# Kernel optimization log

Measured on AMD Instinct MI355X. Metric: run time of the kernel, lower is better.

The kernel has to match this reference:

```python
import jax, jax.numpy as jnp
import numpy as np

D_MODEL = 1024
N_HEADS = 16
HEAD_DIM = D_MODEL // N_HEADS
N_EXPERTS = 8
TOP_K = 2
D_FF = 4096
B, T = 4, 1024
EPS = 1e-5


def setup_inputs() -> dict:
    key = jax.random.key(0)
    ks = jax.random.split(key, 12)
    s = lambda fan_in: 1.0 / np.sqrt(fan_in)
    x = jax.random.normal(ks[0], (B, T, D_MODEL), dtype=jnp.float32)
    # additive causal mask (0 on/below diagonal, -inf above)
    mask = jnp.where(jnp.tril(jnp.ones((T, T), dtype=bool)), 0.0, -1e9).astype(jnp.float32)
    return {
        "x": x,
        "mask": mask,
        "ln1_g": jnp.ones((D_MODEL,), jnp.float32),
        "ln1_b": jnp.zeros((D_MODEL,), jnp.float32),
        "w_qkv": jax.random.normal(ks[1], (D_MODEL, 3 * D_MODEL), jnp.float32) * s(D_MODEL),
        "w_proj": jax.random.normal(ks[2], (D_MODEL, D_MODEL), jnp.float32) * s(D_MODEL),
        "b_proj": jnp.zeros((D_MODEL,), jnp.float32),
        "ln2_g": jnp.ones((D_MODEL,), jnp.float32),
        "ln2_b": jnp.zeros((D_MODEL,), jnp.float32),
        "w_router": jax.random.normal(ks[3], (D_MODEL, N_EXPERTS), jnp.float32) * s(D_MODEL),
        "w1": jax.random.normal(ks[4], (N_EXPERTS, D_MODEL, D_FF), jnp.float32) * s(D_MODEL),
        "b1": jnp.zeros((N_EXPERTS, D_FF), jnp.float32),
        "w2": jax.random.normal(ks[5], (N_EXPERTS, D_FF, D_MODEL), jnp.float32) * s(D_FF),
        "b2": jnp.zeros((N_EXPERTS, D_MODEL), jnp.float32),
    }


def _layer_norm(x, g, b):
    mu = jnp.mean(x, axis=-1, keepdims=True)
    var = jnp.var(x, axis=-1, keepdims=True)
    return (x - mu) * jax.lax.rsqrt(var + EPS) * g + b


def _rope(q, k):
    # q, k: [B, H, T, hd]; GPT-NeoX half-split rotary
    t = q.shape[2]
    half = HEAD_DIM // 2
    inv_freq = 1.0 / (10000.0 ** (jnp.arange(0, half, dtype=jnp.float32) / half))
    ang = jnp.arange(t, dtype=jnp.float32)[:, None] * inv_freq[None, :]  # [T, half]
    cos = jnp.concatenate([jnp.cos(ang), jnp.cos(ang)], axis=-1)[None, None]  # [1,1,T,hd]
    sin = jnp.concatenate([jnp.sin(ang), jnp.sin(ang)], axis=-1)[None, None]

    def rot_half(u):
        u1, u2 = jnp.split(u, 2, axis=-1)
        return jnp.concatenate([-u2, u1], axis=-1)

    return q * cos + rot_half(q) * sin, k * cos + rot_half(k) * sin


def _attention(x, mask, w_qkv, w_proj, b_proj):
    b, t, _ = x.shape
    qkv = x @ w_qkv  # [B,T,3D]
    q, k, v = jnp.split(qkv, 3, axis=-1)
    rs = lambda u: u.reshape(b, t, N_HEADS, HEAD_DIM).transpose(0, 2, 1, 3)
    q, k, v = rs(q), rs(k), rs(v)
    q, k = _rope(q, k)
    scale = HEAD_DIM ** -0.5
    scores = jnp.einsum("bhqd,bhkd->bhqk", q, k) * scale + mask
    attn = jax.nn.softmax(scores, axis=-1)
    out = jnp.einsum("bhqk,bhkd->bhqd", attn, v)
    out = out.transpose(0, 2, 1, 3).reshape(b, t, D_MODEL)
    return out @ w_proj + b_proj


def _moe(x, w_router, w1, b1, w2, b2):
    b, t, d = x.shape
    xf = x.reshape(-1, d)  # [N, d]
    logits = xf @ w_router  # [N, E]
    probs = jax.nn.softmax(logits, axis=-1)
    top_v, top_i = jax.lax.top_k(probs, TOP_K)  # [N, k]
    weights = top_v / jnp.sum(top_v, axis=-1, keepdims=True)
    onehot = jax.nn.one_hot(top_i, N_EXPERTS, dtype=xf.dtype)  # [N, k, E]
    gates = jnp.einsum("nk,nke->ne", weights, onehot)  # [N, E]
    # dense grouped-FFN over experts
    h = jax.nn.gelu(jnp.einsum("nd,edf->enf", xf, w1) + b1[:, None, :], approximate=False)
    y = jnp.einsum("enf,efd->end", h, w2) + b2[:, None, :]
    out = jnp.einsum("end,ne->nd", y, gates).reshape(b, t, d)
    # load-balancing aux loss (Switch-style)
    dispatch = jnp.sum(onehot, axis=1)  # [N, E]
    frac = jnp.mean(dispatch, axis=0) / TOP_K
    mean_prob = jnp.mean(probs, axis=0)
    aux = N_EXPERTS * jnp.sum(frac * mean_prob)
    return out, aux


def reference(x, mask, ln1_g, ln1_b, w_qkv, w_proj, b_proj, ln2_g, ln2_b,
              w_router, w1, b1, w2, b2):
    # dropout is identity (eval / p=0)
    x = x + _attention(_layer_norm(x, ln1_g, ln1_b), mask, w_qkv, w_proj, b_proj)
    moe_out, aux = _moe(_layer_norm(x, ln2_g, ln2_b), w_router, w1, b1, w2, b2)
    x = x + moe_out
    return x, aux
```

## Files before the change

kernel.cpp:

```cpp
#include <hip/hip_runtime.h>
#include <math.h>


typedef __bf16 bf16;
typedef __bf16 bf16x8 __attribute__((ext_vector_type(8)));
typedef float  f32x4  __attribute__((ext_vector_type(4)));

#define D_MODEL 1024
#define SEQ     1024
#define NTOK    4096
#define DFF     4096
#define NEXP    8

__device__ __forceinline__ f32x4 mfma16(bf16x8 a, bf16x8 b, f32x4 c) {
  return __builtin_amdgcn_mfma_f32_16x16x32_bf16(a, b, c, 0, 0, 0);
}

__device__ __forceinline__ void async_cp16(void* lds, const void* g) {
  __builtin_amdgcn_global_load_lds(
      (__attribute__((address_space(1))) void*)(void*)g,
      (__attribute__((address_space(3))) void*)lds, 16, 0, 0);
}

__device__ __forceinline__ int swz(int row, int col) {
  return row * 64 + (col ^ (((row ^ (row >> 3)) & 7) << 3));
}

template<bool SPLIT>
__device__ __forceinline__ void gemm_core(
    const bf16* __restrict__ Ahi, const bf16* __restrict__ Alo,
    const bf16* __restrict__ Bhi, const bf16* __restrict__ Blo,
    long aOff0, long aOff1, long bOff0, long bOff1,
    int K, bf16* As, bf16* Bs, f32x4 acc[4][4])
{
  const int tid  = threadIdx.x;
  const int lane = tid & 63, w = tid >> 6;
  const int fr   = lane & 15, quad = lane >> 4;
  const int wm   = w >> 1,    wn   = w & 1;
  bf16* AsD0 = As + (w * 16) * 32;
  bf16* AsD1 = As + (64 + w * 16) * 32;
  bf16* BsD0 = Bs + (w * 16) * 32;
  bf16* BsD1 = Bs + (64 + w * 16) * 32;
  const int nph = SPLIT ? 3 : 1;
  for (int ph = 0; ph < nph; ++ph) {
    const bf16* Ap = (ph == 1) ? Alo : Ahi;
    const bf16* Bp = (ph == 2) ? Blo : Bhi;
    for (int k0 = 0; k0 < K; k0 += 32) {
      async_cp16(AsD0, Ap + aOff0 + k0);
      async_cp16(AsD1, Ap + aOff1 + k0);
      async_cp16(BsD0, Bp + bOff0 + k0);
      async_cp16(BsD1, Bp + bOff1 + k0);
      __syncthreads();
      bf16x8 af[4], bfv[4];
#pragma unroll
      for (int mi = 0; mi < 4; ++mi)
        af[mi] = *(const bf16x8*)&As[(wm * 64 + mi * 16 + fr) * 32 + quad * 8];
#pragma unroll
      for (int ni = 0; ni < 4; ++ni)
        bfv[ni] = *(const bf16x8*)&Bs[(wn * 64 + ni * 16 + fr) * 32 + quad * 8];
#pragma unroll
      for (int mi = 0; mi < 4; ++mi)
#pragma unroll
        for (int ni = 0; ni < 4; ++ni)
          acc[mi][ni] = mfma16(af[mi], bfv[ni], acc[mi][ni]);
      __syncthreads();
    }
  }
}

__global__ void k_transpose_cast(const float* __restrict__ in,
                                 bf16* __restrict__ oh, bf16* __restrict__ ol,
                                 int K, int N)
{
  const long zo = (long)blockIdx.z * K * N;
  __shared__ float tile[32][33];
  const int tx = threadIdx.x & 31, ty = threadIdx.x >> 5;
  const int r0 = blockIdx.y * 32, c0 = blockIdx.x * 32;
#pragma unroll
  for (int j = 0; j < 4; ++j)
    tile[ty + 8 * j][tx] = in[zo + (long)(r0 + ty + 8 * j) * N + (c0 + tx)];
  __syncthreads();
#pragma unroll
  for (int j = 0; j < 4; ++j) {
    float v = tile[tx][ty + 8 * j];
    long  o = zo + (long)(c0 + ty + 8 * j) * K + (r0 + tx);
    bf16 hh = (bf16)v;
    oh[o] = hh;
    if (ol) ol[o] = (bf16)(v - (float)hh);
  }
}

__global__ __launch_bounds__(256) void k_layernorm(
    const float* __restrict__ x, const float* __restrict__ g,
    const float* __restrict__ b, bf16* __restrict__ oh, bf16* __restrict__ ol)
{
  const int tok = blockIdx.x, tid = threadIdx.x;
  const float4 v = ((const float4*)(x + (long)tok * D_MODEL))[tid];
  float s  = v.x + v.y + v.z + v.w;
  float s2 = v.x * v.x + v.y * v.y + v.z * v.z + v.w * v.w;
#pragma unroll
  for (int off = 1; off < 64; off <<= 1) {
    s  += __shfl_xor(s, off);
    s2 += __shfl_xor(s2, off);
  }
  __shared__ float red[8];
  if ((tid & 63) == 0) { red[tid >> 6] = s; red[4 + (tid >> 6)] = s2; }
  __syncthreads();
  s  = red[0] + red[1] + red[2] + red[3];
  s2 = red[4] + red[5] + red[6] + red[7];
  const float mu   = s * (1.0f / D_MODEL);
  const float var  = s2 * (1.0f / D_MODEL) - mu * mu;
  const float rstd = 1.0f / sqrtf(var + 1e-5f);
  const float4 gg = ((const float4*)g)[tid];
  const float4 bb = ((const float4*)b)[tid];
  float o0 = (v.x - mu) * rstd * gg.x + bb.x;
  float o1 = (v.y - mu) * rstd * gg.y + bb.y;
  float o2 = (v.z - mu) * rstd * gg.z + bb.z;
  float o3 = (v.w - mu) * rstd * gg.w + bb.w;
  const long base = (long)tok * D_MODEL + tid * 4;
  bf16 h0 = (bf16)o0, h1 = (bf16)o1, h2 = (bf16)o2, h3 = (bf16)o3;
  oh[base + 0] = h0; oh[base + 1] = h1; oh[base + 2] = h2; oh[base + 3] = h3;
  if (ol) {
    ol[base + 0] = (bf16)(o0 - (float)h0);
    ol[base + 1] = (bf16)(o1 - (float)h1);
    ol[base + 2] = (bf16)(o2 - (float)h2);
    ol[base + 3] = (bf16)(o3 - (float)h3);
  }
}

__global__ __launch_bounds__(256, 2) void k_gemm_qkv(
    const bf16* __restrict__ Ah, const bf16* __restrict__ Al,
    const bf16* __restrict__ Bh, const bf16* __restrict__ Bl,
    float* __restrict__ out)
{
  __shared__ __align__(16) bf16 As[128 * 32];
  __shared__ __align__(16) bf16 Bs[128 * 32];
  const int tid = threadIdx.x, lane = tid & 63, w = tid >> 6;
  const int fr = lane & 15, quad = lane >> 4;
  const int wm = w >> 1, wn = w & 1;
  const int m0 = blockIdx.y * 128, n0 = blockIdx.x * 128;
  const int lrow = w * 16 + (lane >> 2), colk = (lane & 3) * 8;
  long aOff0 = (long)(m0 + lrow) * D_MODEL + colk;
  long aOff1 = aOff0 + 64L * D_MODEL;
  long bOff0 = (long)(n0 + lrow) * D_MODEL + colk;
  long bOff1 = bOff0 + 64L * D_MODEL;
  f32x4 acc[4][4];
  f32x4 zv = {0.f, 0.f, 0.f, 0.f};
#pragma unroll
  for (int i = 0; i < 4; ++i)
#pragma unroll
    for (int j = 0; j < 4; ++j) acc[i][j] = zv;
  gemm_core<true>(Ah, Al, Bh, Bl, aOff0, aOff1, bOff0, bOff1, D_MODEL, As, Bs, acc);
#pragma unroll
  for (int mi = 0; mi < 4; ++mi)
#pragma unroll
    for (int ni = 0; ni < 4; ++ni) {
      const int col = n0 + wn * 64 + ni * 16 + fr;
#pragma unroll
      for (int r = 0; r < 4; ++r) {
        const int row = m0 + wm * 64 + mi * 16 + quad * 4 + r;
        out[(long)row * 3072 + col] = acc[mi][ni][r];
      }
    }
}

__global__ __launch_bounds__(256) void k_rope(
    const float* __restrict__ qkv,
    bf16* __restrict__ qh, bf16* __restrict__ ql,
    bf16* __restrict__ kh, bf16* __restrict__ kl,
    bf16* __restrict__ vh, bf16* __restrict__ vl)
{
  const int tok = blockIdx.x;
  const int t = tok & (SEQ - 1), bb = tok >> 10;
  const int tid = threadIdx.x;
  const float ft = (float)t;
  for (int it = tid; it < 512; it += 256) {
    const int hh = it >> 5, i = it & 31;
    const float inv = powf(10000.0f, -(float)i * (1.0f / 32.0f));
    const float ang = ft * inv;
    float sn, cs;
    sincosf(ang, &sn, &cs);
    const long src = (long)tok * 3072 + hh * 64 + i;
    const float q0 = qkv[src], q1 = qkv[src + 32];
    const float k0 = qkv[src + 1024], k1 = qkv[src + 1024 + 32];
    const float qo0 = q0 * cs - q1 * sn, qo1 = q1 * cs + q0 * sn;
    const float ko0 = k0 * cs - k1 * sn, ko1 = k1 * cs + k0 * sn;
    const long dst = ((long)(bb * 16 + hh) * SEQ + t) * 64 + i;
    bf16 x;
    x = (bf16)qo0; qh[dst] = x;      ql[dst] = (bf16)(qo0 - (float)x);
    x = (bf16)qo1; qh[dst + 32] = x; ql[dst + 32] = (bf16)(qo1 - (float)x);
    x = (bf16)ko0; kh[dst] = x;      kl[dst] = (bf16)(ko0 - (float)x);
    x = (bf16)ko1; kh[dst + 32] = x; kl[dst + 32] = (bf16)(ko1 - (float)x);
  }
  for (int it = tid; it < 1024; it += 256) {
    const int hh = it >> 6, d = it & 63;
    const float vv = qkv[(long)tok * 3072 + 2048 + it];
    const long dst = ((long)(bb * 16 + hh) * SEQ + t) * 64 + d;
    bf16 x = (bf16)vv;
    vh[dst] = x; vl[dst] = (bf16)(vv - (float)x);
  }
}

__global__ __launch_bounds__(256, 3) void k_flash(
    const bf16* __restrict__ qh, const bf16* __restrict__ ql,
    const bf16* __restrict__ kh, const bf16* __restrict__ kl,
    const bf16* __restrict__ vh, const bf16* __restrict__ vl,
    bf16* __restrict__ oh, bf16* __restrict__ ol)
{
  const int qt = blockIdx.x, bhid = blockIdx.y;
  const int tid = threadIdx.x, lane = tid & 63, w = tid >> 6;
  const int fr = lane & 15, quad = lane >> 4;
  __shared__ __align__(16) bf16 QP0[64 * 64];
  __shared__ __align__(16) bf16 QP1[64 * 64];
  __shared__ __align__(16) bf16 Kh[64 * 64], Kl[64 * 64];
  __shared__ __align__(16) bf16 Vh[64 * 64], Vl[64 * 64];

  const long qbase = ((long)bhid * SEQ + qt * 64) * 64;
  for (int c = tid; c < 512; c += 256) {
    const int row = c >> 3, c8 = (c & 7) << 3;
    *(uint4*)&QP0[swz(row, c8)] = *(const uint4*)&qh[qbase + row * 64 + c8];
    *(uint4*)&QP1[swz(row, c8)] = *(const uint4*)&ql[qbase + row * 64 + c8];
  }
  __syncthreads();
  bf16x8 aQh[2], aQl[2];
#pragma unroll
  for (int kk = 0; kk < 2; ++kk) {
    aQh[kk] = *(const bf16x8*)&QP0[swz(w * 16 + fr, kk * 32 + quad * 8)];
    aQl[kk] = *(const bf16x8*)&QP1[swz(w * 16 + fr, kk * 32 + quad * 8)];
  }
  f32x4 o[4];
  f32x4 zv = {0.f, 0.f, 0.f, 0.f};
#pragma unroll
  for (int ct = 0; ct < 4; ++ct) o[ct] = zv;
  float m_r[4], l_r[4];
#pragma unroll
  for (int r = 0; r < 4; ++r) { m_r[r] = -1e30f; l_r[r] = 0.f; }

  for (int kt = 0; kt <= qt; ++kt) {
    __syncthreads();
    const long kbase = ((long)bhid * SEQ + kt * 64) * 64;
    for (int c = tid; c < 512; c += 256) {
      const int row = c >> 3, c8 = (c & 7) << 3;
      *(uint4*)&Kh[swz(row, c8)] = *(const uint4*)&kh[kbase + row * 64 + c8];
      *(uint4*)&Kl[swz(row, c8)] = *(const uint4*)&kl[kbase + row * 64 + c8];
      uint4 uh = *(const uint4*)&vh[kbase + row * 64 + c8];
      uint4 ul = *(const uint4*)&vl[kbase + row * 64 + c8];
      const bf16* vph = (const bf16*)&uh;
      const bf16* vpl = (const bf16*)&ul;
#pragma unroll
      for (int j = 0; j < 8; ++j) {
        Vh[swz(c8 + j, row)] = vph[j];
        Vl[swz(c8 + j, row)] = vpl[j];
      }
    }
    __syncthreads();

    f32x4 s[4];
#pragma unroll
    for (int nt = 0; nt < 4; ++nt) s[nt] = zv;
#pragma unroll
    for (int nt = 0; nt < 4; ++nt)
#pragma unroll
      for (int kk = 0; kk < 2; ++kk) {
        bf16x8 bh8 = *(const bf16x8*)&Kh[swz(nt * 16 + fr, kk * 32 + quad * 8)];
        bf16x8 bl8 = *(const bf16x8*)&Kl[swz(nt * 16 + fr, kk * 32 + quad * 8)];
        s[nt] = mfma16(aQh[kk], bh8, s[nt]);
        s[nt] = mfma16(aQl[kk], bh8, s[nt]);
        s[nt] = mfma16(aQh[kk], bl8, s[nt]);
      }
    const int qloc = w * 16 + quad * 4;
#pragma unroll
    for (int nt = 0; nt < 4; ++nt)
#pragma unroll
      for (int r = 0; r < 4; ++r) {
        float sv = s[nt][r] * 0.125f;
        if (kt == qt && (nt * 16 + fr) > (qloc + r)) sv = -1e30f;
        s[nt][r] = sv;
      }
    float al4[4];
#pragma unroll
    for (int r = 0; r < 4; ++r) {
      float m = fmaxf(fmaxf(s[0][r], s[1][r]), fmaxf(s[2][r], s[3][r]));
#pragma unroll
      for (int off = 1; off < 16; off <<= 1) m = fmaxf(m, __shfl_xor(m, off));
      const float mn = fmaxf(m_r[r], m);
      al4[r] = expf(m_r[r] - mn);
      m_r[r] = mn;
    }
    float pmat[4][4], ls4[4];
#pragma unroll
    for (int r = 0; r < 4; ++r) ls4[r] = 0.f;
#pragma unroll
    for (int nt = 0; nt < 4; ++nt)
#pragma unroll
      for (int r = 0; r < 4; ++r) {
        const float p = expf(s[nt][r] - m_r[r]);
        pmat[nt][r] = p;
        ls4[r] += p;
      }
#pragma unroll
    for (int r = 0; r < 4; ++r) {
      float l = ls4[r];
#pragma unroll
      for (int off = 1; off < 16; off <<= 1) l += __shfl_xor(l, off);
      l_r[r] = l_r[r] * al4[r] + l;
      o[0][r] *= al4[r]; o[1][r] *= al4[r]; o[2][r] *= al4[r]; o[3][r] *= al4[r];
    }
    bf16* Pw0 = QP0 + w * 1024;
    bf16* Pw1 = QP1 + w * 1024;
#pragma unroll
    for (int nt = 0; nt < 4; ++nt)
#pragma unroll
      for (int r = 0; r < 4; ++r) {
        const float p = pmat[nt][r];
        bf16 hh2 = (bf16)p;
        Pw0[swz(quad * 4 + r, nt * 16 + fr)] = hh2;
        Pw1[swz(quad * 4 + r, nt * 16 + fr)] = (bf16)(p - (float)hh2);
      }
    __syncthreads();
#pragma unroll
    for (int kk = 0; kk < 2; ++kk) {
      bf16x8 aPh = *(const bf16x8*)&Pw0[swz(fr, kk * 32 + quad * 8)];
      bf16x8 aPl = *(const bf16x8*)&Pw1[swz(fr, kk * 32 + quad * 8)];
#pragma unroll
      for (int ct = 0; ct < 4; ++ct) {
        bf16x8 bVh = *(const bf16x8*)&Vh[swz(ct * 16 + fr, kk * 32 + quad * 8)];
        bf16x8 bVl = *(const bf16x8*)&Vl[swz(ct * 16 + fr, kk * 32 + quad * 8)];
        o[ct] = mfma16(aPh, bVh, o[ct]);
        o[ct] = mfma16(aPl, bVh, o[ct]);
        o[ct] = mfma16(aPh, bVl, o[ct]);
      }
    }
  }
  const int b_ = bhid >> 4, h_ = bhid & 15;
#pragma unroll
  for (int ct = 0; ct < 4; ++ct)
#pragma unroll
    for (int r = 0; r < 4; ++r) {
      const int tokn = b_ * SEQ + qt * 64 + w * 16 + quad * 4 + r;
      const int col = h_ * 64 + ct * 16 + fr;
      const float val = o[ct][r] / l_r[r];
      bf16 hh3 = (bf16)val;
      oh[(long)tokn * D_MODEL + col] = hh3;
      ol[(long)tokn * D_MODEL + col] = (bf16)(val - (float)hh3);
    }
}

__global__ __launch_bounds__(256, 2) void k_gemm_proj(
    const bf16* __restrict__ Ah, const bf16* __restrict__ Al,
    const bf16* __restrict__ Bh, const bf16* __restrict__ Bl,
    const float* __restrict__ bproj, const float* __restrict__ xin,
    float* __restrict__ out)
{
  __shared__ __align__(16) bf16 As[128 * 32];
  __shared__ __align__(16) bf16 Bs[128 * 32];
  const int tid = threadIdx.x, lane = tid & 63, w = tid >> 6;
  const int fr = lane & 15, quad = lane >> 4;
  const int wm = w >> 1, wn = w & 1;
  const int m0 = blockIdx.y * 128, n0 = blockIdx.x * 128;
  const int lrow = w * 16 + (lane >> 2), colk = (lane & 3) * 8;
  long aOff0 = (long)(m0 + lrow) * D_MODEL + colk;
  long aOff1 = aOff0 + 64L * D_MODEL;
  long bOff0 = (long)(n0 + lrow) * D_MODEL + colk;
  long bOff1 = bOff0 + 64L * D_MODEL;
  f32x4 acc[4][4];
  f32x4 zv = {0.f, 0.f, 0.f, 0.f};
#pragma unroll
  for (int i = 0; i < 4; ++i)
#pragma unroll
    for (int j = 0; j < 4; ++j) acc[i][j] = zv;
  gemm_core<true>(Ah, Al, Bh, Bl, aOff0, aOff1, bOff0, bOff1, D_MODEL, As, Bs, acc);
#pragma unroll
  for (int mi = 0; mi < 4; ++mi)
#pragma unroll
    for (int ni = 0; ni < 4; ++ni) {
      const int col = n0 + wn * 64 + ni * 16 + fr;
#pragma unroll
      for (int r = 0; r < 4; ++r) {
        const int row = m0 + wm * 64 + mi * 16 + quad * 4 + r;
        out[(long)row * D_MODEL + col] =
            acc[mi][ni][r] + bproj[col] + xin[(long)row * D_MODEL + col];
      }
    }
}

__global__ __launch_bounds__(256) void k_router(
    const float* __restrict__ x1, const float* __restrict__ g,
    const float* __restrict__ b, const float* __restrict__ wr,
    int2* __restrict__ topi, float2* __restrict__ topg,
    float* __restrict__ pbuf)
{
  const int tok = blockIdx.x, tid = threadIdx.x;
  const float4 v = ((const float4*)(x1 + (long)tok * D_MODEL))[tid];
  float s  = v.x + v.y + v.z + v.w;
  float s2 = v.x * v.x + v.y * v.y + v.z * v.z + v.w * v.w;
#pragma unroll
  for (int off = 1; off < 64; off <<= 1) {
    s  += __shfl_xor(s, off);
    s2 += __shfl_xor(s2, off);
  }
  __shared__ float red[8];
  __shared__ float lr[4][8];
  if ((tid & 63) == 0) { red[tid >> 6] = s; red[4 + (tid >> 6)] = s2; }
  __syncthreads();
  s  = red[0] + red[1] + red[2] + red[3];
  s2 = red[4] + red[5] + red[6] + red[7];
  const float mu   = s * (1.0f / D_MODEL);
  const float var  = s2 * (1.0f / D_MODEL) - mu * mu;
  const float rstd = 1.0f / sqrtf(var + 1e-5f);
  const float4 gg = ((const float4*)g)[tid];
  const float4 bb = ((const float4*)b)[tid];
  float n4[4];
  n4[0] = (v.x - mu) * rstd * gg.x + bb.x;
  n4[1] = (v.y - mu) * rstd * gg.y + bb.y;
  n4[2] = (v.z - mu) * rstd * gg.z + bb.z;
  n4[3] = (v.w - mu) * rstd * gg.w + bb.w;
  float part[8];
#pragma unroll
  for (int e = 0; e < 8; ++e) part[e] = 0.f;
  const float* wrow = wr + (long)tid * 4 * 8;
#pragma unroll
  for (int c = 0; c < 4; ++c)
#pragma unroll
    for (int e = 0; e < 8; ++e) part[e] += n4[c] * wrow[c * 8 + e];
#pragma unroll
  for (int off = 1; off < 64; off <<= 1)
#pragma unroll
    for (int e = 0; e < 8; ++e) part[e] += __shfl_xor(part[e], off);
  if ((tid & 63) == 0)
#pragma unroll
    for (int e = 0; e < 8; ++e) lr[tid >> 6][e] = part[e];
  __syncthreads();
  if (tid == 0) {
    float lg[8];
#pragma unroll
    for (int e = 0; e < 8; ++e) lg[e] = lr[0][e] + lr[1][e] + lr[2][e] + lr[3][e];
    float mx = lg[0];
#pragma unroll
    for (int e = 1; e < 8; ++e) mx = fmaxf(mx, lg[e]);
    float pe[8], ssum = 0.f;
#pragma unroll
    for (int e = 0; e < 8; ++e) { pe[e] = expf(lg[e] - mx); ssum += pe[e]; }
    const float inv = 1.0f / ssum;
    int i1 = -1, i2 = -1;
    float v1 = -1.f, v2 = -1.f;
#pragma unroll
    for (int e = 0; e < 8; ++e) {
      const float p = pe[e] * inv;
      pbuf[(long)tok * 8 + e] = p;
      if (p > v1)      { v2 = v1; i2 = i1; v1 = p; i1 = e; }
      else if (p > v2) { v2 = p; i2 = e; }
    }
    const float wsum = v1 + v2;
    topi[tok] = make_int2(i1, i2);
    topg[tok] = make_float2(v1 / wsum, v2 / wsum);
  }
}

__global__ __launch_bounds__(256) void k_scatter(
    const int2* __restrict__ topi,
    int* __restrict__ ecnt, int* __restrict__ perm, int2* __restrict__ pos)
{
  __shared__ int hcnt[NEXP];
  __shared__ int hbase[NEXP];
  const int tid = threadIdx.x;
  const int tok = blockIdx.x * 256 + tid;
  if (tid < NEXP) hcnt[tid] = 0;
  __syncthreads();
  const int2 ti = topi[tok];
  const int r1 = atomicAdd(&hcnt[ti.x], 1);
  const int r2 = atomicAdd(&hcnt[ti.y], 1);
  __syncthreads();
  if (tid < NEXP) hbase[tid] = atomicAdd(&ecnt[tid], hcnt[tid]);
  __syncthreads();
  const int p1 = hbase[ti.x] + r1;
  perm[ti.x * NTOK + p1] = tok;
  const int p2 = hbase[ti.y] + r2;
  perm[ti.y * NTOK + p2] = tok;
  pos[tok] = make_int2(p1, p2);
}

__global__ __launch_bounds__(256) void k_finalize(
    const int* __restrict__ ecnt, const float* __restrict__ pbuf,
    int* __restrict__ eoff, float* __restrict__ aux_out)
{
  __shared__ float partial[256];
  const int tid = threadIdx.x;
  const int e = tid & 7, i0 = tid >> 3;
  float sum = 0.f;
  for (int i = i0; i < NTOK; i += 32) sum += pbuf[(long)i * 8 + e];
  partial[tid] = sum;
  __syncthreads();
  if (tid < 8) {
    float ps = 0.f;
#pragma unroll
    for (int j = 0; j < 32; ++j) ps += partial[j * 8 + tid];
    partial[tid] = ps;
  }
  __syncthreads();
  if (tid == 0) {
    int off = 0;
    float aux = 0.f;
    for (int e2 = 0; e2 < 8; ++e2) {
      eoff[e2] = off;
      off += (ecnt[e2] + 127) & ~127;
      aux += ((float)ecnt[e2] * (1.0f / (NTOK * 2.0f))) * (partial[e2] * (1.0f / NTOK));
    }
    aux_out[0] = 8.0f * aux;
  }
}

__global__ __launch_bounds__(256, 2) void k_gemm_ffn1(
    const bf16* __restrict__ A, const bf16* __restrict__ w1t,
    const float* __restrict__ b1, const int* __restrict__ ecnt,
    const int* __restrict__ eoff, const int* __restrict__ perm,
    bf16* __restrict__ h)
{
  const int e = blockIdx.y >> 5, mt = blockIdx.y & 31;
  const int cnt = ecnt[e];
  if (mt * 128 >= cnt) return;
  __shared__ __align__(16) bf16 As[128 * 32];
  __shared__ __align__(16) bf16 Bs[128 * 32];
  const int tid = threadIdx.x, lane = tid & 63, w = tid >> 6;
  const int fr = lane & 15, quad = lane >> 4;
  const int wm = w >> 1, wn = w & 1;
  const int n0 = blockIdx.x * 128;
  const int lrow = w * 16 + (lane >> 2), colk = (lane & 3) * 8;
  int i0 = mt * 128 + lrow;
  int i1 = i0 + 64;
  i0 = min(i0, cnt - 1);
  i1 = min(i1, cnt - 1);
  const int* pe = perm + e * NTOK;
  long aOff0 = (long)pe[i0] * D_MODEL + colk;
  long aOff1 = (long)pe[i1] * D_MODEL + colk;
  const bf16* B = w1t + (long)e * DFF * D_MODEL;
  long bOff0 = (long)(n0 + lrow) * D_MODEL + colk;
  long bOff1 = bOff0 + 64L * D_MODEL;
  f32x4 acc[4][4];
  f32x4 zv = {0.f, 0.f, 0.f, 0.f};
#pragma unroll
  for (int i = 0; i < 4; ++i)
#pragma unroll
    for (int j = 0; j < 4; ++j) acc[i][j] = zv;
  gemm_core<false>(A, A, B, B, aOff0, aOff1, bOff0, bOff1, D_MODEL, As, Bs, acc);
  const int hbase = eoff[e] + mt * 128;
#pragma unroll
  for (int mi = 0; mi < 4; ++mi)
#pragma unroll
    for (int ni = 0; ni < 4; ++ni) {
      const int col = n0 + wn * 64 + ni * 16 + fr;
#pragma unroll
      for (int r = 0; r < 4; ++r) {
        const int irow = wm * 64 + mi * 16 + quad * 4 + r;
        const float vv = acc[mi][ni][r] + b1[e * DFF + col];
        const float ge = 0.5f * vv * (1.0f + erff(vv * 0.70710678118654752f));
        h[(long)(hbase + irow) * DFF + col] = (bf16)ge;
      }
    }
}

__global__ __launch_bounds__(256, 2) void k_gemm_ffn2(
    const bf16* __restrict__ hbuf, const bf16* __restrict__ w2t,
    const float* __restrict__ b2, const int* __restrict__ ecnt,
    const int* __restrict__ eoff, float* __restrict__ ybuf)
{
  const int e = blockIdx.y >> 5, mt = blockIdx.y & 31;
  const int cnt = ecnt[e];
  if (mt * 128 >= cnt) return;
  __shared__ __align__(16) bf16 As[128 * 32];
  __shared__ __align__(16) bf16 Bs[128 * 32];
  const int tid = threadIdx.x, lane = tid & 63, w = tid >> 6;
  const int fr = lane & 15, quad = lane >> 4;
  const int wm = w >> 1, wn = w & 1;
  const int n0 = blockIdx.x * 128;
  const int lrow = w * 16 + (lane >> 2), colk = (lane & 3) * 8;
  const int rbase = eoff[e] + mt * 128;
  const bf16* A = hbuf + (long)rbase * DFF;
  long aOff0 = (long)lrow * DFF + colk;
  long aOff1 = aOff0 + 64L * DFF;
  const bf16* B = w2t + (long)e * D_MODEL * DFF;
  long bOff0 = (long)(n0 + lrow) * DFF + colk;
  long bOff1 = bOff0 + 64L * DFF;
  f32x4 acc[4][4];
  f32x4 zv = {0.f, 0.f, 0.f, 0.f};
#pragma unroll
  for (int i = 0; i < 4; ++i)
#pragma unroll
    for (int j = 0; j < 4; ++j) acc[i][j] = zv;
  gemm_core<false>(A, A, B, B, aOff0, aOff1, bOff0, bOff1, DFF, As, Bs, acc);
#pragma unroll
  for (int mi = 0; mi < 4; ++mi)
#pragma unroll
    for (int ni = 0; ni < 4; ++ni) {
      const int col = n0 + wn * 64 + ni * 16 + fr;
      const float bias = b2[e * D_MODEL + col];
#pragma unroll
      for (int r = 0; r < 4; ++r) {
        const int irow = wm * 64 + mi * 16 + quad * 4 + r;
        ybuf[(long)(rbase + irow) * D_MODEL + col] = acc[mi][ni][r] + bias;
      }
    }
}

__global__ __launch_bounds__(256) void k_combine(
    const int2* __restrict__ topi, const float2* __restrict__ topg,
    const int2* __restrict__ pos, const int* __restrict__ eoff,
    const float* __restrict__ ybuf, float* __restrict__ out)
{
  const int tok = blockIdx.x, tid = threadIdx.x;
  const int2 ti = topi[tok];
  const int2 pp = pos[tok];
  const float2 tg = topg[tok];
  const long r1 = (long)eoff[ti.x] + pp.x;
  const long r2 = (long)eoff[ti.y] + pp.y;
  const float4 y1 = ((const float4*)(ybuf + r1 * D_MODEL))[tid];
  const float4 y2 = ((const float4*)(ybuf + r2 * D_MODEL))[tid];
  float4* po = (float4*)(out + (long)tok * D_MODEL) + tid;
  float4 o = *po;
  o.x += tg.x * y1.x + tg.y * y2.x;
  o.y += tg.x * y1.y + tg.y * y2.y;
  o.z += tg.x * y1.z + tg.y * y2.z;
  o.w += tg.x * y1.w + tg.y * y2.w;
  *po = o;
}

extern "C" void kernel_launch(void* const* d_in, const int* in_sizes, int n_in,
                              void* d_out, int out_size, void* d_ws, size_t ws_size,
                              hipStream_t stream) {
  const float* x     = (const float*)d_in[0];
  const float* ln1g  = (const float*)d_in[2];
  const float* ln1b  = (const float*)d_in[3];
  const float* wqkv  = (const float*)d_in[4];
  const float* wproj = (const float*)d_in[5];
  const float* bproj = (const float*)d_in[6];
  const float* ln2g  = (const float*)d_in[7];
  const float* ln2b  = (const float*)d_in[8];
  const float* wrout = (const float*)d_in[9];
  const float* w1    = (const float*)d_in[10];
  const float* b1    = (const float*)d_in[11];
  const float* w2    = (const float*)d_in[12];
  const float* b2    = (const float*)d_in[13];
  float* out = (float*)d_out;

  char* p = (char*)d_ws;
  auto alloc = [&](size_t n) { char* r = p; p += (n + 255) & ~(size_t)255; return r; };

  bf16* wqkvT_h = (bf16*)alloc(3072L * 1024 * 2);
  bf16* wqkvT_l = (bf16*)alloc(3072L * 1024 * 2);
  bf16* wprojT_h = (bf16*)alloc(1024L * 1024 * 2);
  bf16* wprojT_l = (bf16*)alloc(1024L * 1024 * 2);
  bf16* w1T = (bf16*)alloc(8L * 4096 * 1024 * 2);
  bf16* w2T = (bf16*)alloc(8L * 1024 * 4096 * 2);
  bf16* ln_h = (bf16*)alloc(4096L * 1024 * 2);
  bf16* ln_l = (bf16*)alloc(4096L * 1024 * 2);
  bf16* attn_h = (bf16*)alloc(4096L * 1024 * 2);
  bf16* attn_l = (bf16*)alloc(4096L * 1024 * 2);
  int*   perm  = (int*)alloc(8L * 4096 * 4);
  int2*  topi  = (int2*)alloc(4096L * 8);
  float2* topg = (float2*)alloc(4096L * 8);
  int2*  pos   = (int2*)alloc(4096L * 8);
  float* pbuf  = (float*)alloc(4096L * 8 * 4);
  char*  ctrl  = alloc(256);
  int*   ecnt  = (int*)ctrl;
  int*   eoff  = (int*)(ctrl + 64);
  float* ybuf  = (float*)alloc(9216L * 1024 * 4);
  char* big = alloc(100663296);
  float* qkvf = (float*)big;
  bf16* qh = (bf16*)(big + 50331648);
  bf16* ql = qh + 4194304;
  bf16* kh = ql + 4194304;
  bf16* kl = kh + 4194304;
  bf16* vh = kl + 4194304;
  bf16* vl = vh + 4194304;
  bf16* hbuf = (bf16*)big;

  dim3 blk(256);

  k_transpose_cast<<<dim3(3072 / 32, 1024 / 32, 1), blk, 0, stream>>>(wqkv, wqkvT_h, wqkvT_l, 1024, 3072);
  k_transpose_cast<<<dim3(1024 / 32, 1024 / 32, 1), blk, 0, stream>>>(wproj, wprojT_h, wprojT_l, 1024, 1024);
  k_transpose_cast<<<dim3(4096 / 32, 1024 / 32, 8), blk, 0, stream>>>(w1, w1T, nullptr, 1024, 4096);
  k_transpose_cast<<<dim3(1024 / 32, 4096 / 32, 8), blk, 0, stream>>>(w2, w2T, nullptr, 4096, 1024);
  hipMemsetAsync(ctrl, 0, 256, stream);

  k_layernorm<<<4096, blk, 0, stream>>>(x, ln1g, ln1b, ln_h, ln_l);
  k_gemm_qkv<<<dim3(24, 32), blk, 0, stream>>>(ln_h, ln_l, wqkvT_h, wqkvT_l, qkvf);
  k_rope<<<4096, blk, 0, stream>>>(qkvf, qh, ql, kh, kl, vh, vl);
  k_flash<<<dim3(16, 64), blk, 0, stream>>>(qh, ql, kh, kl, vh, vl, attn_h, attn_l);
  k_gemm_proj<<<dim3(8, 32), blk, 0, stream>>>(attn_h, attn_l, wprojT_h, wprojT_l, bproj, x, out);

  k_layernorm<<<4096, blk, 0, stream>>>(out, ln2g, ln2b, ln_h, nullptr);
  k_router<<<4096, blk, 0, stream>>>(out, ln2g, ln2b, wrout, topi, topg, pbuf);
  k_scatter<<<16, blk, 0, stream>>>(topi, ecnt, perm, pos);
  k_finalize<<<1, blk, 0, stream>>>(ecnt, pbuf, eoff, out + 4194304);
  k_gemm_ffn1<<<dim3(32, 256), blk, 0, stream>>>(ln_h, w1T, b1, ecnt, eoff, perm, hbuf);
  k_gemm_ffn2<<<dim3(8, 256), blk, 0, stream>>>(hbuf, w2T, b2, ecnt, eoff, ybuf);
  k_combine<<<4096, blk, 0, stream>>>(topi, topg, pos, eoff, ybuf, out);
}
```

Before: 1.058 ms.

## Double-buffer GEMM LDS tiles and split-K the FFN2 expert GEMM

The shared GEMM core now uses two LDS buffers and issues the async global-to-LDS loads for the next k-step before computing the current one, with one barrier per step instead of two. This is meant to hide global load latency behind MFMA work, at the cost of doubling LDS per block. Separately, the FFN2 expert GEMM is split along K into two halves over a z grid dimension, writing partial sums to two y buffers that the combine kernel adds. That raises FFN2 parallelism for its long K=4096 loop but doubles y buffer memory and combine-kernel reads.

Measured after the change: 1.047 ms. No clear change (-1.0%).

```diff
diff --git a/kernel.cpp b/kernel.cpp
--- a/kernel.cpp
+++ b/kernel.cpp
@@ -11,6 +11,7 @@
 #define NTOK    4096
 #define DFF     4096
 #define NEXP    8
+#define YSTRIDE (9216L * 1024)
 
 __device__ __forceinline__ f32x4 mfma16(bf16x8 a, bf16x8 b, f32x4 c) {
   return __builtin_amdgcn_mfma_f32_16x16x32_bf16(a, b, c, 0, 0, 0);
@@ -37,34 +38,45 @@
   const int lane = tid & 63, w = tid >> 6;
   const int fr   = lane & 15, quad = lane >> 4;
   const int wm   = w >> 1,    wn   = w & 1;
-  bf16* AsD0 = As + (w * 16) * 32;
-  bf16* AsD1 = As + (64 + w * 16) * 32;
-  bf16* BsD0 = Bs + (w * 16) * 32;
-  bf16* BsD1 = Bs + (64 + w * 16) * 32;
-  const int nph = SPLIT ? 3 : 1;
-  for (int ph = 0; ph < nph; ++ph) {
+  const int ldst0 = (w * 16) * 32;
+  const int ldst1 = (64 + w * 16) * 32;
+  const int ksteps = K >> 5;
+  const int nsteps = (SPLIT ? 3 : 1) * ksteps;
+
+  auto stage = [&](int s, int buf) {
+    const int ph = SPLIT ? (s / ksteps) : 0;
+    const int k0 = (SPLIT ? (s - ph * ksteps) : s) << 5;
     const bf16* Ap = (ph == 1) ? Alo : Ahi;
     const bf16* Bp = (ph == 2) ? Blo : Bhi;
-    for (int k0 = 0; k0 < K; k0 += 32) {
-      async_cp16(AsD0, Ap + aOff0 + k0);
-      async_cp16(AsD1, Ap + aOff1 + k0);
-      async_cp16(BsD0, Bp + bOff0 + k0);
-      async_cp16(BsD1, Bp + bOff1 + k0);
-      __syncthreads();
-      bf16x8 af[4], bfv[4];
-#pragma unroll
-      for (int mi = 0; mi < 4; ++mi)
-        af[mi] = *(const bf16x8*)&As[(wm * 64 + mi * 16 + fr) * 32 + quad * 8];
+    bf16* Ab = As + buf * (128 * 32);
+    bf16* Bb = Bs + buf * (128 * 32);
+    async_cp16(Ab + ldst0, Ap + aOff0 + k0);
+    async_cp16(Ab + ldst1, Ap + aOff1 + k0);
+    async_cp16(Bb + ldst0, Bp + bOff0 + k0);
+    async_cp16(Bb + ldst1, Bp + bOff1 + k0);
+  };
+
+  stage(0, 0);
+  __syncthreads();
+  int cur = 0;
+  for (int s = 0; s < nsteps; ++s) {
+    if (s + 1 < nsteps) stage(s + 1, cur ^ 1);
+    const bf16* Ab = As + cur * (128 * 32);
+    const bf16* Bb = Bs + cur * (128 * 32);
+    bf16x8 af[4], bfv[4];
+#pragma unroll
+    for (int mi = 0; mi < 4; ++mi)
+      af[mi] = *(const bf16x8*)&Ab[(wm * 64 + mi * 16 + fr) * 32 + quad * 8];
+#pragma unroll
+    for (int ni = 0; ni < 4; ++ni)
+      bfv[ni] = *(const bf16x8*)&Bb[(wn * 64 + ni * 16 + fr) * 32 + quad * 8];
+#pragma unroll
+    for (int mi = 0; mi < 4; ++mi)
 #pragma unroll
       for (int ni = 0; ni < 4; ++ni)
-        bfv[ni] = *(const bf16x8*)&Bs[(wn * 64 + ni * 16 + fr) * 32 + quad * 8];
-#pragma unroll
-      for (int mi = 0; mi < 4; ++mi)
-#pragma unroll
-        for (int ni = 0; ni < 4; ++ni)
-          acc[mi][ni] = mfma16(af[mi], bfv[ni], acc[mi][ni]);
-      __syncthreads();
-    }
+        acc[mi][ni] = mfma16(af[mi], bfv[ni], acc[mi][ni]);
+    __syncthreads();
+    cur ^= 1;
   }
 }
 
@@ -133,8 +145,8 @@
     const bf16* __restrict__ Bh, const bf16* __restrict__ Bl,
     float* __restrict__ out)
 {
-  __shared__ __align__(16) bf16 As[128 * 32];
-  __shared__ __align__(16) bf16 Bs[128 * 32];
+  __shared__ __align__(16) bf16 As[2 * 128 * 32];
+  __shared__ __align__(16) bf16 Bs[2 * 128 * 32];
   const int tid = threadIdx.x, lane = tid & 63, w = tid >> 6;
   const int fr = lane & 15, quad = lane >> 4;
   const int wm = w >> 1, wn = w & 1;
@@ -352,8 +364,8 @@
     const float* __restrict__ bproj, const float* __restrict__ xin,
     float* __restrict__ out)
 {
-  __shared__ __align__(16) bf16 As[128 * 32];
-  __shared__ __align__(16) bf16 Bs[128 * 32];
+  __shared__ __align__(16) bf16 As[2 * 128 * 32];
+  __shared__ __align__(16) bf16 Bs[2 * 128 * 32];
   const int tid = threadIdx.x, lane = tid & 63, w = tid >> 6;
   const int fr = lane & 15, quad = lane >> 4;
   const int wm = w >> 1, wn = w & 1;
@@ -519,8 +531,8 @@
   const int e = blockIdx.y >> 5, mt = blockIdx.y & 31;
   const int cnt = ecnt[e];
   if (mt * 128 >= cnt) return;
-  __shared__ __align__(16) bf16 As[128 * 32];
-  __shared__ __align__(16) bf16 Bs[128 * 32];
+  __shared__ __align__(16) bf16 As[2 * 128 * 32];
+  __shared__ __align__(16) bf16 Bs[2 * 128 * 32];
   const int tid = threadIdx.x, lane = tid & 63, w = tid >> 6;
   const int fr = lane & 15, quad = lane >> 4;
   const int wm = w >> 1, wn = w & 1;
@@ -567,19 +579,21 @@
   const int e = blockIdx.y >> 5, mt = blockIdx.y & 31;
   const int cnt = ecnt[e];
   if (mt * 128 >= cnt) return;
-  __shared__ __align__(16) bf16 As[128 * 32];
-  __shared__ __align__(16) bf16 Bs[128 * 32];
+  __shared__ __align__(16) bf16 As[2 * 128 * 32];
+  __shared__ __align__(16) bf16 Bs[2 * 128 * 32];
   const int tid = threadIdx.x, lane = tid & 63, w = tid >> 6;
   const int fr = lane & 15, quad = lane >> 4;
   const int wm = w >> 1, wn = w & 1;
   const int n0 = blockIdx.x * 128;
+  const int z = blockIdx.z;
+  const long kOff = (long)z * (DFF / 2);
   const int lrow = w * 16 + (lane >> 2), colk = (lane & 3) * 8;
   const int rbase = eoff[e] + mt * 128;
   const bf16* A = hbuf + (long)rbase * DFF;
-  long aOff0 = (long)lrow * DFF + colk;
+  long aOff0 = (long)lrow * DFF + colk + kOff;
   long aOff1 = aOff0 + 64L * DFF;
   const bf16* B = w2t + (long)e * D_MODEL * DFF;
-  long bOff0 = (long)(n0 + lrow) * DFF + colk;
+  long bOff0 = (long)(n0 + lrow) * DFF + colk + kOff;
   long bOff1 = bOff0 + 64L * DFF;
   f32x4 acc[4][4];
   f32x4 zv = {0.f, 0.f, 0.f, 0.f};
@@ -587,17 +601,18 @@
   for (int i = 0; i < 4; ++i)
 #pragma unroll
     for (int j = 0; j < 4; ++j) acc[i][j] = zv;
-  gemm_core<false>(A, A, B, B, aOff0, aOff1, bOff0, bOff1, DFF, As, Bs, acc);
+  gemm_core<false>(A, A, B, B, aOff0, aOff1, bOff0, bOff1, DFF / 2, As, Bs, acc);
+  float* yb = ybuf + (long)z * YSTRIDE;
 #pragma unroll
   for (int mi = 0; mi < 4; ++mi)
 #pragma unroll
     for (int ni = 0; ni < 4; ++ni) {
       const int col = n0 + wn * 64 + ni * 16 + fr;
-      const float bias = b2[e * D_MODEL + col];
+      const float bias = (z == 0) ? b2[e * D_MODEL + col] : 0.0f;
 #pragma unroll
       for (int r = 0; r < 4; ++r) {
         const int irow = wm * 64 + mi * 16 + quad * 4 + r;
-        ybuf[(long)(rbase + irow) * D_MODEL + col] = acc[mi][ni][r] + bias;
+        yb[(long)(rbase + irow) * D_MODEL + col] = acc[mi][ni][r] + bias;
       }
     }
 }
@@ -613,14 +628,16 @@
   const float2 tg = topg[tok];
   const long r1 = (long)eoff[ti.x] + pp.x;
   const long r2 = (long)eoff[ti.y] + pp.y;
-  const float4 y1 = ((const float4*)(ybuf + r1 * D_MODEL))[tid];
-  const float4 y2 = ((const float4*)(ybuf + r2 * D_MODEL))[tid];
+  const float4 y1a = ((const float4*)(ybuf + r1 * D_MODEL))[tid];
+  const float4 y1b = ((const float4*)(ybuf + YSTRIDE + r1 * D_MODEL))[tid];
+  const float4 y2a = ((const float4*)(ybuf + r2 * D_MODEL))[tid];
+  const float4 y2b = ((const float4*)(ybuf + YSTRIDE + r2 * D_MODEL))[tid];
   float4* po = (float4*)(out + (long)tok * D_MODEL) + tid;
   float4 o = *po;
-  o.x += tg.x * y1.x + tg.y * y2.x;
-  o.y += tg.x * y1.y + tg.y * y2.y;
-  o.z += tg.x * y1.z + tg.y * y2.z;
-  o.w += tg.x * y1.w + tg.y * y2.w;
+  o.x += tg.x * (y1a.x + y1b.x) + tg.y * (y2a.x + y2b.x);
+  o.y += tg.x * (y1a.y + y1b.y) + tg.y * (y2a.y + y2b.y);
+  o.z += tg.x * (y1a.z + y1b.z) + tg.y * (y2a.z + y2b.z);
+  o.w += tg.x * (y1a.w + y1b.w) + tg.y * (y2a.w + y2b.w);
   *po = o;
 }
 
@@ -663,7 +680,7 @@
   char*  ctrl  = alloc(256);
   int*   ecnt  = (int*)ctrl;
   int*   eoff  = (int*)(ctrl + 64);
-  float* ybuf  = (float*)alloc(9216L * 1024 * 4);
+  float* ybuf  = (float*)alloc(2L * YSTRIDE * 4);
   char* big = alloc(100663296);
   float* qkvf = (float*)big;
   bf16* qh = (bf16*)(big + 50331648);
@@ -693,6 +710,6 @@
   k_scatter<<<16, blk, 0, stream>>>(topi, ecnt, perm, pos);
   k_finalize<<<1, blk, 0, stream>>>(ecnt, pbuf, eoff, out + 4194304);
   k_gemm_ffn1<<<dim3(32, 256), blk, 0, stream>>>(ln_h, w1T, b1, ecnt, eoff, perm, hbuf);
-  k_gemm_ffn2<<<dim3(8, 256), blk, 0, stream>>>(hbuf, w2T, b2, ecnt, eoff, ybuf);
+  k_gemm_ffn2<<<dim3(8, 256, 2), blk, 0, stream>>>(hbuf, w2T, b2, ecnt, eoff, ybuf);
   k_combine<<<4096, blk, 0, stream>>>(topi, topg, pos, eoff, ybuf, out);
 }
```
